# Performance work log

Measured on AMD Instinct MI355X. Metric: run time of the kernel, lower is better.

Reference implementation:

```python
import jax, jax.numpy as jnp
import numpy as np
import math

N = 100000; NFEAT = 500; M = 512; HIDDEN = 128; NLAYER = 2; K = 10; NCLASS = 40; ALPHA = 0.1


def setup_inputs() -> dict:
    key = jax.random.key(0)
    ks = jax.random.split(key, 20)
    s_in = 1.0 / math.sqrt(NFEAT); s_h = 1.0 / math.sqrt(HIDDEN); s_e = 1.0 / math.sqrt(HIDDEN + 1)
    kvec = jnp.arange(K + 1, dtype=jnp.float32)
    fW = ALPHA * (1.0 - ALPHA) ** kvec
    fW = fW.at[-1].set((1.0 - ALPHA) ** K)
    return {
        "x": jax.random.normal(ks[0], (N, NFEAT), jnp.float32),
        "e0": jax.random.uniform(ks[1], (M,), jnp.float32) * 2.0,
        "e1": jax.random.uniform(ks[2], (M,), jnp.float32) * 2.0,
        "u0": jax.random.normal(ks[3], (N, M), jnp.float32) / math.sqrt(N),
        "u1": jax.random.normal(ks[4], (N, M), jnp.float32) / math.sqrt(N),
        "fe_w1": jax.random.uniform(ks[5], (NFEAT, HIDDEN), jnp.float32, -s_in, s_in),
        "fe_b1": jnp.zeros((HIDDEN,), jnp.float32),
        "fe_w2": jax.random.uniform(ks[6], (HIDDEN, HIDDEN), jnp.float32, -s_h, s_h),
        "fe_b2": jnp.zeros((HIDDEN,), jnp.float32),
        "eig_w": jax.random.uniform(ks[7], (HIDDEN + 1, 1), jnp.float32, -s_e, s_e),
        "eig_b": jnp.zeros((1,), jnp.float32),
        "layer_weight": 0.01 * jax.random.normal(ks[8], (NLAYER, 2, HIDDEN), jnp.float32),
        "ln_gamma": jnp.ones((NLAYER, HIDDEN), jnp.float32),
        "ln_beta": jnp.zeros((NLAYER, HIDDEN), jnp.float32),
        "fW": fW,
        "att0": jax.random.uniform(ks[9], (HIDDEN, 1), jnp.float32, -1.0, 1.0),
        "att1": jax.random.uniform(ks[10], (HIDDEN, 1), jnp.float32, -1.0, 1.0),
        "att2": jax.random.uniform(ks[11], (HIDDEN, 1), jnp.float32, -1.0, 1.0),
        "att_vec": jax.random.uniform(ks[12], (3, 3), jnp.float32, -1.0 / math.sqrt(3.0), 1.0 / math.sqrt(3.0)),
        "lin3_w": jax.random.uniform(ks[13], (HIDDEN, NCLASS), jnp.float32, -s_h, s_h),
        "lin3_b": jnp.zeros((NCLASS,), jnp.float32),
    }


def _fourier_encode(e, eig_w, eig_b):
    # e: [m] -> [m, 1]; constant-1 column then cos(k*pi*e), k=1..HIDDEN
    freqs = jnp.arange(1, HIDDEN + 1, dtype=e.dtype)
    eeig = jnp.concatenate([jnp.ones((e.shape[0], 1), e.dtype),
                            jnp.cos(math.pi * e[:, None] * freqs)], axis=1)
    return eeig @ eig_w + eig_b  # [m, 1]


def _mfnn_layer(feats, w, g, b):
    # feats: [N, 2, H]; weight [2, H] -> sum over bases, LayerNorm, ReLU
    h = jnp.sum(feats * w, axis=1)
    mu = jnp.mean(h, axis=-1, keepdims=True)
    var = jnp.var(h, axis=-1, keepdims=True)
    h = (h - mu) * jax.lax.rsqrt(var + 1e-5) * g + b
    return jax.nn.relu(h)


def reference(x, e0, e1, u0, u1, fe_w1, fe_b1, fe_w2, fe_b2, eig_w, eig_b,
              layer_weight, ln_gamma, ln_beta, fW, att0, att1, att2, att_vec,
              lin3_w, lin3_b):
    h = jax.nn.relu(x @ fe_w1 + fe_b1) @ fe_w2 + fe_b2  # feat_encoder (dropouts are eval no-ops)
    result = [h]
    tail = jnp.sum(fW[1:])  # r is invariant across the K inner steps: hidden = fW[0]*h + sum(fW[1:])*r
    for e_i, u_i in ((e0, u0), (e1, u1)):
        eig = _fourier_encode(e_i, eig_w, eig_b)  # [m, 1]
        for L in range(NLAYER):
            utx = u_i.T @ h                # [m, H]
            r = u_i @ (eig * utx)          # [N, H] spectral propagation
            hidden = h * fW[0] + tail * r
            feats = jnp.stack([h, hidden], axis=1)  # [N, 2, H]
            h = _mfnn_layer(feats, layer_weight[L], ln_gamma[L], ln_beta[L])
        result.append(h)
    logits = jax.nn.sigmoid(jnp.concatenate(
        [result[0] @ att0, result[1] @ att1, result[2] @ att2], axis=1)) @ att_vec
    att = jax.nn.softmax(logits, axis=1)  # [N, 3]
    h = att[:, 0:1] * result[0] + att[:, 1:2] * result[1] + att[:, 2:3] * result[2]
    return jax.nn.log_softmax(h @ lin3_w + lin3_b, axis=1)
```

## Files before the change

kernel.cpp:

```cpp
#include <hip/hip_runtime.h>
#include <stdint.h>

#define NR 100000L
#define KC 92
#define CHN 1088L

typedef __attribute__((ext_vector_type(8))) short s16x8;
typedef __attribute__((ext_vector_type(4))) short s16x4;
typedef __attribute__((ext_vector_type(4))) float f32x4;

__device__ __forceinline__ unsigned short f2bf(float f) {
  union { float f; unsigned u; } v; v.f = f;
  unsigned r = v.u + 0x7FFFu + ((v.u >> 16) & 1u);
  return (unsigned short)(r >> 16);
}
__device__ __forceinline__ float bf2f(unsigned short s) {
  union { unsigned u; float f; } v; v.u = ((unsigned)s) << 16;
  return v.f;
}
__device__ __forceinline__ f32x4 MF(s16x8 a, s16x8 b, f32x4 c) {
  return __builtin_amdgcn_mfma_f32_16x16x32_bf16(a, b, c, 0, 0, 0);
}

__device__ __forceinline__ int swz(int row, int col) {
  return row * 64 + (((col >> 3) ^ (row & 7)) << 3) + (col & 7);
}

__device__ __forceinline__ void gld16(const void* g, void* l) {
  __builtin_amdgcn_global_load_lds(
      (const __attribute__((address_space(1))) void*)g,
      (__attribute__((address_space(3))) void*)l, 16, 0, 0);
}

template<int ROWS>
__device__ __forceinline__ void stage_async(unsigned short* lds, const unsigned short* src,
    long pitch, long r0, long k0, int tid) {
  const int lane = tid & 63, w = tid >> 6;
  const int lr = lane >> 3, lc = lane & 7;
#pragma unroll
  for (int it = 0; it < ROWS / 32; ++it) {
    const int rowbase = w * (ROWS / 4) + it * 8;
    const int row = rowbase + lr;
    const int sc = lc ^ (row & 7);
    gld16(src + (r0 + row) * pitch + k0 + sc * 8, lds + rowbase * 64);
  }
}

template<int ROWS>
__device__ __forceinline__ void stage_guard(unsigned short* lds, const unsigned short* src,
    long pitch, long r0, long rlim, long k0, long klim, int tid) {
  const int f8 = tid & 7;
#pragma unroll
  for (int it = 0; it < ROWS / 32; ++it) {
    const int row = (tid >> 3) + it * 32;
    const long gr = r0 + row, gk = k0 + f8 * 8;
    s16x8 v = {};
    if (gr < rlim && gk < klim) v = *(const s16x8*)(src + gr * pitch + gk);
    *(s16x8*)(lds + row * 64 + ((f8 ^ (row & 7)) << 3)) = v;
  }
}

template<int ROWS>
__device__ __forceinline__ void stage_guard_f32(unsigned short* lds, const float* src,
    long pitch, long r0, long rlim, long k0, long klim, int tid) {
  const int f4 = tid & 15;
#pragma unroll
  for (int it = 0; it < ROWS / 16; ++it) {
    const int row = (tid >> 4) + it * 16;
    const long gr = r0 + row, gk = k0 + f4 * 4;
    f32x4 v = {};
    if (gr < rlim && gk < klim) v = *(const f32x4*)(src + gr * pitch + gk);
    s16x4 o;
    o[0] = (short)f2bf(v[0]); o[1] = (short)f2bf(v[1]);
    o[2] = (short)f2bf(v[2]); o[3] = (short)f2bf(v[3]);
    const int c = f4 >> 1, h = f4 & 1;
    *(s16x4*)(lds + row * 64 + ((c ^ (row & 7)) << 3) + h * 4) = o;
  }
}

__device__ __forceinline__ void stage_utr_f32(unsigned short* lds, const float* u,
    long n0, long m0, int tid) {
  const int mm = tid & 63;
  const int base = tid >> 6;
#pragma unroll
  for (int it = 0; it < 16; ++it) {
    const int nl = base + it * 4;
    const long n = n0 + nl;
    unsigned short v = 0;
    if (n < NR) v = f2bf(u[n * 512 + m0 + mm]);
    lds[swz(mm, nl)] = v;
  }
}

__device__ __forceinline__ s16x8 fragA(const unsigned short* lds, int row, int kk, int lane) {
  const int c = kk * 4 + (lane >> 4);
  return *(const s16x8*)(lds + row * 64 + ((c ^ (row & 7)) << 3));
}

__global__ void k_prep(const float* __restrict__ e0, const float* __restrict__ e1,
    const float* __restrict__ fe_w1, const float* __restrict__ fe_w2,
    const float* __restrict__ eig_w, const float* __restrict__ eig_b,
    const float* __restrict__ lw, const float* __restrict__ fW,
    unsigned short* __restrict__ W1T, unsigned short* __restrict__ W2T,
    float* __restrict__ eig, float* __restrict__ coef) {
  long id = (long)blockIdx.x * 256 + threadIdx.x;
  if (id < 65536) {
    int j = (int)(id >> 9), k = (int)(id & 511);
    W1T[id] = (k < 500) ? f2bf(fe_w1[(long)k * 128 + j]) : (unsigned short)0;
  } else if (id < 65536 + 16384) {
    long q = id - 65536; int j = (int)(q >> 7), k = (int)(q & 127);
    W2T[q] = f2bf(fe_w2[(long)k * 128 + j]);
  } else if (id < 65536 + 16384 + 1024) {
    long q = id - 65536 - 16384; int b = (int)(q >> 9), m = (int)(q & 511);
    const float* e = b ? e1 : e0;
    float s = eig_b[0] + eig_w[0];
    float pe = 3.14159265358979323846f * e[m];
    for (int f = 1; f <= 128; ++f) s += cosf(pe * (float)f) * eig_w[f];
    eig[q] = s;
  } else if (id < 65536 + 16384 + 1024 + 256) {
    long q = id - 65536 - 16384 - 1024; int L = (int)(q >> 7), j = (int)(q & 127);
    float tail = 0.f;
    for (int k = 1; k <= 10; ++k) tail += fW[k];
    float w0 = lw[L * 256 + j], w1 = lw[L * 256 + 128 + j];
    coef[L * 256 + j] = w0 + fW[0] * w1;
    coef[L * 256 + 128 + j] = tail * w1;
  }
}

__global__ __launch_bounds__(256) void k_cvtx(const float* __restrict__ x,
    unsigned short* __restrict__ xb) {
  const long t = (long)blockIdx.x * 256 + threadIdx.x;
  const int k4 = (int)(t & 127) * 4;
  const long n = t >> 7;
  s16x4 o = {};
  if (k4 < 500) {
    f32x4 v = *(const f32x4*)(x + n * 500 + k4);
    o[0] = (short)f2bf(v[0]); o[1] = (short)f2bf(v[1]);
    o[2] = (short)f2bf(v[2]); o[3] = (short)f2bf(v[3]);
  }
  *(s16x4*)(xb + n * 512 + k4) = o;
}

__global__ __launch_bounds__(256) void k_cvtT(const float* __restrict__ u,
    unsigned short* __restrict__ Ubf, unsigned short* __restrict__ UbT) {
  __shared__ float T[64 * 64];
  const int tid = threadIdx.x;
  const int nt = blockIdx.x >> 3, mt = blockIdx.x & 7;
  const long n0 = (long)nt * 64, m0 = (long)mt * 64;
  const int r = tid >> 3;
  const int c8 = (tid & 7) * 8;
  const int u0 = c8 >> 2;
#pragma unroll
  for (int p = 0; p < 2; ++p) {
    const int rr = r + p * 32;
    const long n = n0 + rr;
    f32x4 a = {}, b = {};
    if (n < NR) {
      a = *(const f32x4*)(u + n * 512 + m0 + c8);
      b = *(const f32x4*)(u + n * 512 + m0 + c8 + 4);
    }
    const int sw = (rr >> 3) & 7;
    *(f32x4*)&T[rr * 64 + ((u0 ^ sw) << 2)] = a;
    *(f32x4*)&T[rr * 64 + (((u0 + 1) ^ sw) << 2)] = b;
    if (n < NR) {
      s16x8 o;
      o[0] = (short)f2bf(a[0]); o[1] = (short)f2bf(a[1]);
      o[2] = (short)f2bf(a[2]); o[3] = (short)f2bf(a[3]);
      o[4] = (short)f2bf(b[0]); o[5] = (short)f2bf(b[1]);
      o[6] = (short)f2bf(b[2]); o[7] = (short)f2bf(b[3]);
      *(s16x8*)(Ubf + n * 512 + m0 + c8) = o;
    }
  }
  __syncthreads();
  const int nb8 = (tid & 7) * 8;
  const int sw2 = tid & 7;
#pragma unroll
  for (int p = 0; p < 2; ++p) {
    const int mm = r + p * 32;
    const int mu = mm >> 2, ml = mm & 3;
    s16x8 o;
#pragma unroll
    for (int e = 0; e < 8; ++e)
      o[e] = (short)f2bf(T[(nb8 + e) * 64 + (((mu) ^ sw2) << 2) + ml]);
    const long nb = n0 + nb8;
    if (nb + 7 < NR) {
      *(s16x8*)(UbT + (long)(m0 + mm) * NR + nb) = o;
    } else {
#pragma unroll
      for (int e = 0; e < 8; ++e)
        if (nb + e < NR) UbT[(long)(m0 + mm) * NR + nb + e] = o[e];
    }
  }
}

__global__ __launch_bounds__(256) void k_gemm1(const unsigned short* __restrict__ xb,
    const unsigned short* __restrict__ W1T, const float* __restrict__ b1,
    unsigned short* __restrict__ t) {
  __shared__ __align__(16) unsigned short Al[128 * 64];
  __shared__ __align__(16) unsigned short Bl[128 * 64];
  const int tid = threadIdx.x, lane = tid & 63, w = tid >> 6;
  const long n0 = (long)blockIdx.x * 128;
  const bool edge = (n0 + 128) > NR;
  f32x4 acc[2][8] = {};
  for (int kt = 0; kt < 8; ++kt) {
    if (!edge) stage_async<128>(Al, xb, 512, n0, kt * 64L, tid);
    else       stage_guard<128>(Al, xb, 512, n0, NR, kt * 64L, 512, tid);
    stage_async<128>(Bl, W1T, 512, 0, kt * 64L, tid);
    __syncthreads();
#pragma unroll
    for (int kk = 0; kk < 2; ++kk) {
      s16x8 af0 = fragA(Al, w * 32 + (lane & 15), kk, lane);
      s16x8 af1 = fragA(Al, w * 32 + 16 + (lane & 15), kk, lane);
#pragma unroll
      for (int ct = 0; ct < 8; ++ct) {
        s16x8 bfr = fragA(Bl, ct * 16 + (lane & 15), kk, lane);
        acc[0][ct] = MF(af0, bfr, acc[0][ct]);
        acc[1][ct] = MF(af1, bfr, acc[1][ct]);
      }
    }
    __syncthreads();
  }
  const int cl = lane & 15, g = lane >> 4;
#pragma unroll
  for (int ct = 0; ct < 8; ++ct) {
    const int j = ct * 16 + cl;
    const float bias = b1[j];
#pragma unroll
    for (int rt = 0; rt < 2; ++rt)
#pragma unroll
      for (int r = 0; r < 4; ++r) {
        const long n = n0 + w * 32 + rt * 16 + (g << 2) + r;
        if (n < NR) {
          float v = acc[rt][ct][r] + bias;
          t[n * 128 + j] = f2bf(v > 0.f ? v : 0.f);
        }
      }
  }
}

__global__ __launch_bounds__(256) void k_gemm1f(const float* __restrict__ x,
    const unsigned short* __restrict__ W1T, const float* __restrict__ b1,
    unsigned short* __restrict__ t) {
  __shared__ __align__(16) unsigned short Al[64 * 64];
  __shared__ __align__(16) unsigned short Bl[128 * 64];
  const int tid = threadIdx.x, lane = tid & 63, w = tid >> 6;
  const long n0 = (long)blockIdx.x * 64;
  f32x4 acc[8] = {};
  for (int kt = 0; kt < 8; ++kt) {
    stage_guard_f32<64>(Al, x, 500, n0, NR, kt * 64L, 500, tid);
    stage_guard<128>(Bl, W1T, 512, 0, 1L << 40, kt * 64L, 512, tid);
    __syncthreads();
#pragma unroll
    for (int kk = 0; kk < 2; ++kk) {
      s16x8 af = fragA(Al, (w << 4) + (lane & 15), kk, lane);
#pragma unroll
      for (int ct = 0; ct < 8; ++ct) {
        s16x8 bfr = fragA(Bl, (ct << 4) + (lane & 15), kk, lane);
        acc[ct] = MF(af, bfr, acc[ct]);
      }
    }
    __syncthreads();
  }
  const int cl = lane & 15, g = lane >> 4;
#pragma unroll
  for (int ct = 0; ct < 8; ++ct) {
    int j = (ct << 4) + cl;
    float bias = b1[j];
#pragma unroll
    for (int r = 0; r < 4; ++r) {
      long n = n0 + (w << 4) + (g << 2) + r;
      if (n < NR) {
        float v = acc[ct][r] + bias;
        t[n * 128 + j] = f2bf(v > 0.f ? v : 0.f);
      }
    }
  }
}

__global__ __launch_bounds__(256) void k_gemm2(const unsigned short* __restrict__ W2T,
    const unsigned short* __restrict__ t, const float* __restrict__ b2,
    unsigned short* __restrict__ hT) {
  __shared__ __align__(16) unsigned short Al[128 * 64];
  __shared__ __align__(16) unsigned short Bl[128 * 64];
  const int tid = threadIdx.x, lane = tid & 63, w = tid >> 6;
  const long n0 = (long)blockIdx.x * 128;
  const bool edge = (n0 + 128) > NR;
  f32x4 acc[8][2] = {};
  for (int kt = 0; kt < 2; ++kt) {
    stage_async<128>(Al, W2T, 128, 0, kt * 64L, tid);
    if (!edge) stage_async<128>(Bl, t, 128, n0, kt * 64L, tid);
    else       stage_guard<128>(Bl, t, 128, n0, NR, kt * 64L, 128, tid);
    __syncthreads();
#pragma unroll
    for (int kk = 0; kk < 2; ++kk) {
      s16x8 bf0 = fragA(Bl, w * 32 + (lane & 15), kk, lane);
      s16x8 bf1 = fragA(Bl, w * 32 + 16 + (lane & 15), kk, lane);
#pragma unroll
      for (int rt = 0; rt < 8; ++rt) {
        s16x8 af = fragA(Al, rt * 16 + (lane & 15), kk, lane);
        acc[rt][0] = MF(af, bf0, acc[rt][0]);
        acc[rt][1] = MF(af, bf1, acc[rt][1]);
      }
    }
    __syncthreads();
  }
  const int cl = lane & 15, g = lane >> 4;
#pragma unroll
  for (int rt = 0; rt < 8; ++rt)
#pragma unroll
    for (int r = 0; r < 4; ++r) {
      const int j = rt * 16 + (g << 2) + r;
      const float bias = b2[j];
#pragma unroll
      for (int ct = 0; ct < 2; ++ct) {
        const long n = n0 + w * 32 + ct * 16 + cl;
        if (n < NR) hT[(long)j * NR + n] = f2bf(acc[rt][ct][r] + bias);
      }
    }
}

__global__ __launch_bounds__(256, 3) void k_utx(const unsigned short* __restrict__ hT,
    const unsigned short* __restrict__ UbT, unsigned short* __restrict__ P) {
  __shared__ __align__(16) unsigned short Al[128 * 64];
  __shared__ __align__(16) unsigned short Bl[128 * 64];
  const int tid = threadIdx.x, lane = tid & 63, w = tid >> 6;
  const int mt = blockIdx.x & 3, c = blockIdx.x >> 2;
  const long m0 = (long)mt * 128, nb = (long)c * CHN;
  f32x4 acc[8][2] = {};
  for (int kt = 0; kt < 17; ++kt) {
    const long n0 = nb + kt * 64;
    if (n0 + 64 <= NR) {
      stage_async<128>(Al, hT, NR, 0, n0, tid);
      stage_async<128>(Bl, UbT, NR, m0, n0, tid);
    } else {
      stage_guard<128>(Al, hT, NR, 0, 1L << 40, n0, NR, tid);
      stage_guard<128>(Bl, UbT, NR, m0, 1L << 40, n0, NR, tid);
    }
    __syncthreads();
#pragma unroll
    for (int kk = 0; kk < 2; ++kk) {
      s16x8 bf0 = fragA(Bl, w * 32 + (lane & 15), kk, lane);
      s16x8 bf1 = fragA(Bl, w * 32 + 16 + (lane & 15), kk, lane);
#pragma unroll
      for (int rt = 0; rt < 8; ++rt) {
        s16x8 af = fragA(Al, rt * 16 + (lane & 15), kk, lane);
        acc[rt][0] = MF(af, bf0, acc[rt][0]);
        acc[rt][1] = MF(af, bf1, acc[rt][1]);
      }
    }
    __syncthreads();
  }
  const int cl = lane & 15, g = lane >> 4;
  unsigned short* Pc = P + (long)c * 65536;
#pragma unroll
  for (int rt = 0; rt < 8; ++rt)
#pragma unroll
    for (int r = 0; r < 4; ++r) {
      const int j = rt * 16 + (g << 2) + r;
#pragma unroll
      for (int ct = 0; ct < 2; ++ct) {
        const long m = m0 + w * 32 + ct * 16 + cl;
        Pc[(long)j * 512 + m] = f2bf(acc[rt][ct][r]);
      }
    }
}

__global__ __launch_bounds__(256) void k_utx0(const unsigned short* __restrict__ hT,
    const float* __restrict__ u, unsigned short* __restrict__ P) {
  __shared__ __align__(16) unsigned short Al[128 * 64];
  __shared__ __align__(16) unsigned short Bl[64 * 64];
  const int tid = threadIdx.x, lane = tid & 63, w = tid >> 6;
  const int mt = blockIdx.x & 7, c = blockIdx.x >> 3;
  const long m0 = (long)mt * 64, nb = (long)c * CHN;
  f32x4 acc[8] = {};
  for (int kt = 0; kt < 17; ++kt) {
    const long n0 = nb + kt * 64;
    stage_guard<128>(Al, hT, NR, 0, 1L << 40, n0, NR, tid);
    stage_utr_f32(Bl, u, n0, m0, tid);
    __syncthreads();
#pragma unroll
    for (int kk = 0; kk < 2; ++kk) {
      s16x8 bfr = fragA(Bl, (w << 4) + (lane & 15), kk, lane);
#pragma unroll
      for (int rt = 0; rt < 8; ++rt) {
        s16x8 af = fragA(Al, (rt << 4) + (lane & 15), kk, lane);
        acc[rt] = MF(af, bfr, acc[rt]);
      }
    }
    __syncthreads();
  }
  const int cl = lane & 15, g = lane >> 4;
  const long m = m0 + (w << 4) + cl;
  unsigned short* Pc = P + (long)c * 65536;
#pragma unroll
  for (int rt = 0; rt < 8; ++rt)
#pragma unroll
    for (int r = 0; r < 4; ++r) {
      int j = (rt << 4) + (g << 2) + r;
      Pc[(long)j * 512 + m] = f2bf(acc[rt][r]);
    }
}

__global__ void k_reduce(const unsigned short* __restrict__ P, const float* __restrict__ eig,
                         unsigned short* __restrict__ sT) {
  const int t4 = blockIdx.x * 256 + threadIdx.x;
  const int idx = t4 * 4;
  const int m = idx & 511;
  float s0 = 0.f, s1 = 0.f, s2 = 0.f, s3 = 0.f;
  const unsigned short* p = P + idx;
#pragma unroll 4
  for (int c = 0; c < KC; ++c) {
    s16x4 v = *(const s16x4*)(p + (long)c * 65536);
    s0 += bf2f((unsigned short)v[0]); s1 += bf2f((unsigned short)v[1]);
    s2 += bf2f((unsigned short)v[2]); s3 += bf2f((unsigned short)v[3]);
  }
  s16x4 o;
  o[0] = (short)f2bf(s0 * eig[m]);     o[1] = (short)f2bf(s1 * eig[m + 1]);
  o[2] = (short)f2bf(s2 * eig[m + 2]); o[3] = (short)f2bf(s3 * eig[m + 3]);
  *(s16x4*)(sT + idx) = o;
}

__global__ __launch_bounds__(256) void k_rgemm(const unsigned short* __restrict__ sT,
    const unsigned short* __restrict__ Ubf, const unsigned short* __restrict__ hin,
    unsigned short* __restrict__ hout, const float* __restrict__ c0,
    const float* __restrict__ c1, const float* __restrict__ gam,
    const float* __restrict__ bet) {
  __shared__ __align__(16) unsigned short Al[128 * 64];
  __shared__ __align__(16) unsigned short Bl[64 * 64];
  const int tid = threadIdx.x, lane = tid & 63, w = tid >> 6;
  const long n0 = (long)blockIdx.x * 64;
  const bool edge = (n0 + 64) > NR;
  f32x4 acc[8] = {};
  for (int kt = 0; kt < 8; ++kt) {
    stage_async<128>(Al, sT, 512, 0, kt * 64L, tid);
    if (!edge) stage_async<64>(Bl, Ubf, 512, n0, kt * 64L, tid);
    else       stage_guard<64>(Bl, Ubf, 512, n0, NR, kt * 64L, 512, tid);
    __syncthreads();
#pragma unroll
    for (int kk = 0; kk < 2; ++kk) {
      s16x8 bfr = fragA(Bl, (w << 4) + (lane & 15), kk, lane);
#pragma unroll
      for (int rt = 0; rt < 8; ++rt) {
        s16x8 af = fragA(Al, rt * 16 + (lane & 15), kk, lane);
        acc[rt] = MF(af, bfr, acc[rt]);
      }
    }
    __syncthreads();
  }
  if (!edge) stage_async<128>(Al, hin, NR, 0, n0, tid);
  else       stage_guard<128>(Al, hin, NR, 0, 1L << 40, n0, NR, tid);
  __syncthreads();
  const int cl = lane & 15, g = lane >> 4;
  const int nl = (w << 4) + cl;
  float sum = 0.f, ssq = 0.f;
#pragma unroll
  for (int rt = 0; rt < 8; ++rt)
#pragma unroll
    for (int r = 0; r < 4; ++r) {
      const int j = rt * 16 + (g << 2) + r;
      const float hp = bf2f(Al[swz(j, nl)]);
      const float pv = hp * c0[j] + c1[j] * acc[rt][r];
      acc[rt][r] = pv;
      sum += pv; ssq += pv * pv;
    }
  sum += __shfl_xor(sum, 16, 64); sum += __shfl_xor(sum, 32, 64);
  ssq += __shfl_xor(ssq, 16, 64); ssq += __shfl_xor(ssq, 32, 64);
  const float mu = sum * (1.f / 128.f);
  const float rs = rsqrtf(ssq * (1.f / 128.f) - mu * mu + 1e-5f);
  __syncthreads();
#pragma unroll
  for (int rt = 0; rt < 8; ++rt)
#pragma unroll
    for (int r = 0; r < 4; ++r) {
      const int j = rt * 16 + (g << 2) + r;
      float o = (acc[rt][r] - mu) * rs * gam[j] + bet[j];
      Al[swz(j, nl)] = f2bf(o > 0.f ? o : 0.f);
    }
  __syncthreads();
  const int f8 = tid & 7;
  const long gk = n0 + f8 * 8;
#pragma unroll
  for (int it = 0; it < 4; ++it) {
    const int j = (tid >> 3) + it * 32;
    const s16x8 v = *(const s16x8*)(Al + j * 64 + ((f8 ^ (j & 7)) << 3));
    if (gk + 7 < NR) {
      *(s16x8*)(hout + (long)j * NR + gk) = v;
    } else {
#pragma unroll
      for (int e = 0; e < 8; ++e)
        if (gk + e < NR) hout[(long)j * NR + gk + e] = v[e];
    }
  }
}

__global__ __launch_bounds__(256) void k_rgemm64(const unsigned short* __restrict__ sT,
    const float* __restrict__ u, const unsigned short* __restrict__ hin,
    unsigned short* __restrict__ hout, const float* __restrict__ c0,
    const float* __restrict__ c1, const float* __restrict__ gam,
    const float* __restrict__ bet) {
  __shared__ __align__(16) unsigned short Al[128 * 64];
  __shared__ __align__(16) unsigned short Bl[64 * 64];
  const int tid = threadIdx.x, lane = tid & 63, w = tid >> 6;
  const long n0 = (long)blockIdx.x * 64;
  f32x4 acc[8] = {};
  for (int kt = 0; kt < 8; ++kt) {
    stage_guard<128>(Al, sT, 512, 0, 1L << 40, kt * 64L, 512, tid);
    stage_guard_f32<64>(Bl, u, 512, n0, NR, kt * 64L, 512, tid);
    __syncthreads();
#pragma unroll
    for (int kk = 0; kk < 2; ++kk) {
      s16x8 bfr = fragA(Bl, (w << 4) + (lane & 15), kk, lane);
#pragma unroll
      for (int rt = 0; rt < 8; ++rt) {
        s16x8 af = fragA(Al, (rt << 4) + (lane & 15), kk, lane);
        acc[rt] = MF(af, bfr, acc[rt]);
      }
    }
    __syncthreads();
  }
  const int cl = lane & 15, g = lane >> 4;
  const long n = n0 + (w << 4) + cl;
  const bool valid = n < NR;
  float sum = 0.f, ssq = 0.f;
#pragma unroll
  for (int rt = 0; rt < 8; ++rt)
#pragma unroll
    for (int r = 0; r < 4; ++r) {
      int j = (rt << 4) + (g << 2) + r;
      float hp = valid ? bf2f(hin[(long)j * NR + n]) : 0.f;
      float pv = hp * c0[j] + c1[j] * acc[rt][r];
      acc[rt][r] = pv;
      sum += pv; ssq += pv * pv;
    }
  sum += __shfl_xor(sum, 16, 64); sum += __shfl_xor(sum, 32, 64);
  ssq += __shfl_xor(ssq, 16, 64); ssq += __shfl_xor(ssq, 32, 64);
  const float mu = sum * (1.f / 128.f);
  const float rs = rsqrtf(ssq * (1.f / 128.f) - mu * mu + 1e-5f);
  if (valid) {
#pragma unroll
    for (int rt = 0; rt < 8; ++rt)
#pragma unroll
      for (int r = 0; r < 4; ++r) {
        int j = (rt << 4) + (g << 2) + r;
        float o = (acc[rt][r] - mu) * rs * gam[j] + bet[j];
        hout[(long)j * NR + n] = f2bf(o > 0.f ? o : 0.f);
      }
  }
}

__global__ __launch_bounds__(256) void k_final(const unsigned short* __restrict__ R0,
    const unsigned short* __restrict__ R1, const unsigned short* __restrict__ R2,
    const float* __restrict__ att0, const float* __restrict__ att1,
    const float* __restrict__ att2, const float* __restrict__ av,
    const float* __restrict__ W, const float* __restrict__ bias,
    float* __restrict__ out) {
  __shared__ __align__(16) float Wl[128 * 40];
  __shared__ float Av[3][128];
  __shared__ float zb[256 * 41];
  const int tid = threadIdx.x;
  for (int i = tid; i < 5120; i += 256) Wl[i] = W[i];
  if (tid < 128) { Av[0][tid] = att0[tid]; Av[1][tid] = att1[tid]; Av[2][tid] = att2[tid]; }
  __syncthreads();
  const long n0 = (long)blockIdx.x * 256;
  const long n = n0 + tid;
  const long nn = n < NR ? n : NR - 1;
  float a0 = 0.f, a1 = 0.f, a2 = 0.f;
  for (int j = 0; j < 128; ++j) {
    a0 += bf2f(R0[(long)j * NR + nn]) * Av[0][j];
    a1 += bf2f(R1[(long)j * NR + nn]) * Av[1][j];
    a2 += bf2f(R2[(long)j * NR + nn]) * Av[2][j];
  }
  const float s0 = 1.f / (1.f + expf(-a0));
  const float s1 = 1.f / (1.f + expf(-a1));
  const float s2 = 1.f / (1.f + expf(-a2));
  const float l0 = s0 * av[0] + s1 * av[3] + s2 * av[6];
  const float l1 = s0 * av[1] + s1 * av[4] + s2 * av[7];
  const float l2 = s0 * av[2] + s1 * av[5] + s2 * av[8];
  const float mx = fmaxf(l0, fmaxf(l1, l2));
  const float e0v = expf(l0 - mx), e1v = expf(l1 - mx), e2v = expf(l2 - mx);
  const float inv = 1.f / (e0v + e1v + e2v);
  const float w0 = e0v * inv, w1 = e1v * inv, w2 = e2v * inv;
  float z[40];
#pragma unroll
  for (int c = 0; c < 40; ++c) z[c] = bias[c];
  for (int j = 0; j < 128; ++j) {
    const float h = w0 * bf2f(R0[(long)j * NR + nn]) + w1 * bf2f(R1[(long)j * NR + nn])
                  + w2 * bf2f(R2[(long)j * NR + nn]);
#pragma unroll
    for (int c4 = 0; c4 < 10; ++c4) {
      f32x4 wv = *(const f32x4*)(&Wl[j * 40 + c4 * 4]);
      z[c4 * 4 + 0] += h * wv[0];
      z[c4 * 4 + 1] += h * wv[1];
      z[c4 * 4 + 2] += h * wv[2];
      z[c4 * 4 + 3] += h * wv[3];
    }
  }
  float mz = z[0];
#pragma unroll
  for (int c = 1; c < 40; ++c) mz = fmaxf(mz, z[c]);
  float se = 0.f;
#pragma unroll
  for (int c = 0; c < 40; ++c) se += expf(z[c] - mz);
  const float ls = logf(se);
#pragma unroll
  for (int c = 0; c < 40; ++c) zb[tid * 41 + c] = z[c] - mz - ls;
  __syncthreads();
  long rows = NR - n0; if (rows > 256) rows = 256;
  const long cnt = rows * 40;
  for (long i = tid; i < cnt; i += 256)
    out[n0 * 40 + i] = zb[(i / 40) * 41 + (i % 40)];
}

extern "C" void kernel_launch(void* const* d_in, const int* in_sizes, int n_in,
                              void* d_out, int out_size, void* d_ws, size_t ws_size,
                              hipStream_t stream) {
  const float* x      = (const float*)d_in[0];
  const float* e0     = (const float*)d_in[1];
  const float* e1     = (const float*)d_in[2];
  const float* u0     = (const float*)d_in[3];
  const float* u1     = (const float*)d_in[4];
  const float* fe_w1  = (const float*)d_in[5];
  const float* fe_b1  = (const float*)d_in[6];
  const float* fe_w2  = (const float*)d_in[7];
  const float* fe_b2  = (const float*)d_in[8];
  const float* eig_w  = (const float*)d_in[9];
  const float* eig_bi = (const float*)d_in[10];
  const float* lw     = (const float*)d_in[11];
  const float* ln_g   = (const float*)d_in[12];
  const float* ln_b   = (const float*)d_in[13];
  const float* fW     = (const float*)d_in[14];
  const float* att0   = (const float*)d_in[15];
  const float* att1   = (const float*)d_in[16];
  const float* att2   = (const float*)d_in[17];
  const float* attv   = (const float*)d_in[18];
  const float* lin3w  = (const float*)d_in[19];
  const float* lin3b  = (const float*)d_in[20];
  float* out = (float*)d_out;

  const size_t SZ_H = (size_t)NR * 128 * 2;
  const size_t SZ_P = (size_t)KC * 65536 * 2;
  const size_t SZ_U = (size_t)NR * 512 * 2;
  const size_t SZ_X = (size_t)NR * 512 * 2;

  char* p = (char*)d_ws;
  unsigned short* R0T = (unsigned short*)p; p += SZ_H;
  unsigned short* R1T = (unsigned short*)p; p += SZ_H;
  unsigned short* R2T = (unsigned short*)p; p += SZ_H;
  unsigned short* P   = (unsigned short*)p; p += SZ_P;
  unsigned short* W1T = (unsigned short*)p; p += 131072;
  unsigned short* W2T = (unsigned short*)p; p += 32768;
  unsigned short* sT  = (unsigned short*)p; p += 131072;
  float* eig          = (float*)p;          p += 4096;
  float* coef         = (float*)p;          p += 2048;
  const size_t base = (size_t)(p - (char*)d_ws);
  const bool full = ws_size >= base + SZ_X + 2 * SZ_U;
  unsigned short* xb  = nullptr;
  unsigned short* UbT = nullptr;
  unsigned short* Ubf = nullptr;
  if (full) {
    xb  = (unsigned short*)p; p += SZ_X;
    UbT = (unsigned short*)p; p += SZ_U;
    Ubf = (unsigned short*)p; p += SZ_U;
  }

  k_prep<<<325, 256, 0, stream>>>(e0, e1, fe_w1, fe_w2, eig_w, eig_bi, lw, fW,
                                  W1T, W2T, eig, coef);
  const int GB64  = (int)((NR + 63) / 64);
  const int GB128 = (int)((NR + 127) / 128);

  if (full) {
    k_cvtx<<<50000, 256, 0, stream>>>(x, xb);
    k_gemm1<<<GB128, 256, 0, stream>>>(xb, W1T, fe_b1, R1T);
  } else {
    k_gemm1f<<<GB64, 256, 0, stream>>>(x, W1T, fe_b1, R1T);
  }
  k_gemm2<<<GB128, 256, 0, stream>>>(W2T, R1T, fe_b2, R0T);

  for (int b = 0; b < 2; ++b) {
    const float* u = b ? u1 : u0;
    if (full) k_cvtT<<<GB64 * 8, 256, 0, stream>>>(u, Ubf, UbT);
    const unsigned short* hin = (b == 0) ? R0T : R1T;
    unsigned short* hb = b ? R2T : R1T;
    for (int L = 0; L < 2; ++L) {
      unsigned short* hout = hb;
      if (full) k_utx<<<4 * KC, 256, 0, stream>>>(hin, UbT, P);
      else      k_utx0<<<8 * KC, 256, 0, stream>>>(hin, u, P);
      k_reduce<<<64, 256, 0, stream>>>(P, eig + b * 512, sT);
      if (full)
        k_rgemm<<<GB64, 256, 0, stream>>>(sT, Ubf, hin, hout,
            coef + L * 256, coef + L * 256 + 128, ln_g + L * 128, ln_b + L * 128);
      else
        k_rgemm64<<<GB64, 256, 0, stream>>>(sT, u, hin, hout,
            coef + L * 256, coef + L * 256 + 128, ln_g + L * 128, ln_b + L * 128);
      hin = hout;
    }
  }
  k_final<<<(int)((NR + 255) / 256), 256, 0, stream>>>(R0T, R1T, R2T,
      att0, att1, att2, attv, lin3w, lin3b, out);
}
```

Before: 717.1 us.

## Fuse x bf16 conversion into first GEMM and remap utx block order

Drops the separate pass that converted x to a padded bf16 buffer. The first feature GEMM now loads fp32 x directly and converts it while staging, using 128-row tiles. This saves a full write and re-read of a 100 MB intermediate but gives up the async bf16 staging path. The utx kernel also remaps block IDs, probably so neighbouring chunks land on different XCDs for better cache locality.

```diff
diff --git a/kernel.cpp b/kernel.cpp
--- a/kernel.cpp
+++ b/kernel.cpp
@@ -127,20 +127,6 @@
   }
 }
 
-__global__ __launch_bounds__(256) void k_cvtx(const float* __restrict__ x,
-    unsigned short* __restrict__ xb) {
-  const long t = (long)blockIdx.x * 256 + threadIdx.x;
-  const int k4 = (int)(t & 127) * 4;
-  const long n = t >> 7;
-  s16x4 o = {};
-  if (k4 < 500) {
-    f32x4 v = *(const f32x4*)(x + n * 500 + k4);
-    o[0] = (short)f2bf(v[0]); o[1] = (short)f2bf(v[1]);
-    o[2] = (short)f2bf(v[2]); o[3] = (short)f2bf(v[3]);
-  }
-  *(s16x4*)(xb + n * 512 + k4) = o;
-}
-
 __global__ __launch_bounds__(256) void k_cvtT(const float* __restrict__ u,
     unsigned short* __restrict__ Ubf, unsigned short* __restrict__ UbT) {
   __shared__ float T[64 * 64];
@@ -193,18 +179,16 @@
   }
 }
 
-__global__ __launch_bounds__(256) void k_gemm1(const unsigned short* __restrict__ xb,
+__global__ __launch_bounds__(256) void k_gemm1(const float* __restrict__ x,
     const unsigned short* __restrict__ W1T, const float* __restrict__ b1,
     unsigned short* __restrict__ t) {
   __shared__ __align__(16) unsigned short Al[128 * 64];
   __shared__ __align__(16) unsigned short Bl[128 * 64];
   const int tid = threadIdx.x, lane = tid & 63, w = tid >> 6;
   const long n0 = (long)blockIdx.x * 128;
-  const bool edge = (n0 + 128) > NR;
   f32x4 acc[2][8] = {};
   for (int kt = 0; kt < 8; ++kt) {
-    if (!edge) stage_async<128>(Al, xb, 512, n0, kt * 64L, tid);
-    else       stage_guard<128>(Al, xb, 512, n0, NR, kt * 64L, 512, tid);
+    stage_guard_f32<128>(Al, x, 500, n0, NR, kt * 64L, 500, tid);
     stage_async<128>(Bl, W1T, 512, 0, kt * 64L, tid);
     __syncthreads();
 #pragma unroll
@@ -235,45 +219,6 @@
           t[n * 128 + j] = f2bf(v > 0.f ? v : 0.f);
         }
       }
-  }
-}
-
-__global__ __launch_bounds__(256) void k_gemm1f(const float* __restrict__ x,
-    const unsigned short* __restrict__ W1T, const float* __restrict__ b1,
-    unsigned short* __restrict__ t) {
-  __shared__ __align__(16) unsigned short Al[64 * 64];
-  __shared__ __align__(16) unsigned short Bl[128 * 64];
-  const int tid = threadIdx.x, lane = tid & 63, w = tid >> 6;
-  const long n0 = (long)blockIdx.x * 64;
-  f32x4 acc[8] = {};
-  for (int kt = 0; kt < 8; ++kt) {
-    stage_guard_f32<64>(Al, x, 500, n0, NR, kt * 64L, 500, tid);
-    stage_guard<128>(Bl, W1T, 512, 0, 1L << 40, kt * 64L, 512, tid);
-    __syncthreads();
-#pragma unroll
-    for (int kk = 0; kk < 2; ++kk) {
-      s16x8 af = fragA(Al, (w << 4) + (lane & 15), kk, lane);
-#pragma unroll
-      for (int ct = 0; ct < 8; ++ct) {
-        s16x8 bfr = fragA(Bl, (ct << 4) + (lane & 15), kk, lane);
-        acc[ct] = MF(af, bfr, acc[ct]);
-      }
-    }
-    __syncthreads();
-  }
-  const int cl = lane & 15, g = lane >> 4;
-#pragma unroll
-  for (int ct = 0; ct < 8; ++ct) {
-    int j = (ct << 4) + cl;
-    float bias = b1[j];
-#pragma unroll
-    for (int r = 0; r < 4; ++r) {
-      long n = n0 + (w << 4) + (g << 2) + r;
-      if (n < NR) {
-        float v = acc[ct][r] + bias;
-        t[n * 128 + j] = f2bf(v > 0.f ? v : 0.f);
-      }
-    }
   }
 }
 
@@ -324,7 +269,9 @@
   __shared__ __align__(16) unsigned short Al[128 * 64];
   __shared__ __align__(16) unsigned short Bl[128 * 64];
   const int tid = threadIdx.x, lane = tid & 63, w = tid >> 6;
-  const int mt = blockIdx.x & 3, c = blockIdx.x >> 2;
+  const int bid = blockIdx.x;
+  const int logical = (bid & 7) * 46 + (bid >> 3);
+  const int mt = logical & 3, c = logical >> 2;
   const long m0 = (long)mt * 128, nb = (long)c * CHN;
   f32x4 acc[8][2] = {};
   for (int kt = 0; kt < 17; ++kt) {
@@ -640,7 +587,6 @@
   const size_t SZ_H = (size_t)NR * 128 * 2;
   const size_t SZ_P = (size_t)KC * 65536 * 2;
   const size_t SZ_U = (size_t)NR * 512 * 2;
-  const size_t SZ_X = (size_t)NR * 512 * 2;
 
   char* p = (char*)d_ws;
   unsigned short* R0T = (unsigned short*)p; p += SZ_H;
@@ -653,12 +599,10 @@
   float* eig          = (float*)p;          p += 4096;
   float* coef         = (float*)p;          p += 2048;
   const size_t base = (size_t)(p - (char*)d_ws);
-  const bool full = ws_size >= base + SZ_X + 2 * SZ_U;
-  unsigned short* xb  = nullptr;
+  const bool full = ws_size >= base + 2 * SZ_U;
   unsigned short* UbT = nullptr;
   unsigned short* Ubf = nullptr;
   if (full) {
-    xb  = (unsigned short*)p; p += SZ_X;
     UbT = (unsigned short*)p; p += SZ_U;
     Ubf = (unsigned short*)p; p += SZ_U;
   }
@@ -668,12 +612,7 @@
   const int GB64  = (int)((NR + 63) / 64);
   const int GB128 = (int)((NR + 127) / 128);
 
-  if (full) {
-    k_cvtx<<<50000, 256, 0, stream>>>(x, xb);
-    k_gemm1<<<GB128, 256, 0, stream>>>(xb, W1T, fe_b1, R1T);
-  } else {
-    k_gemm1f<<<GB64, 256, 0, stream>>>(x, W1T, fe_b1, R1T);
-  }
+  k_gemm1<<<GB128, 256, 0, stream>>>(x, W1T, fe_b1, R1T);
   k_gemm2<<<GB128, 256, 0, stream>>>(W2T, R1T, fe_b2, R0T);
 
   for (int b = 0; b < 2; ++b) {
```

After: 719.0 us. Within noise of the previous version (+0.3%).
